# Kernel tuning notes

Measured on AMD Instinct MI355X. Metric: run time of the kernel, lower is better.

## Reference

```python
import jax, jax.numpy as jnp
import numpy as np

KH = KW = 3
K = KH * KW
STRIDE = 1
PAD = 1
DIL = 1
DG = 1  # deformable groups


def conv2d(x, w, b):
    out = jax.lax.conv_general_dilated(
        x, w, window_strides=(STRIDE, STRIDE),
        padding=[(PAD, PAD), (PAD, PAD)], rhs_dilation=(DIL, DIL),
        dimension_numbers=('NCHW', 'OIHW', 'NCHW'))
    return out + b[None, :, None, None]


def deform_conv2d(x, offset, mask, w, b):
    """DCNv2: bilinear sample at predicted offsets, modulate by mask, GEMM with w."""
    B, Cin, H, W = x.shape
    Ho, Wo = offset.shape[2], offset.shape[3]
    cpg = Cin // DG
    # torchvision layout: channel 2*(g*K+k) = dy, 2*(g*K+k)+1 = dx
    off = offset.reshape(B, DG, K, 2, Ho, Wo)
    off_y, off_x = off[:, :, :, 0], off[:, :, :, 1]  # [B,DG,K,Ho,Wo]
    m = mask.reshape(B, DG, K, Ho, Wo)
    ky = jnp.repeat(jnp.arange(KH), KW) * DIL          # [K] kernel row offsets
    kx = jnp.tile(jnp.arange(KW), KH) * DIL            # [K] kernel col offsets
    hh = jnp.arange(Ho) * STRIDE - PAD
    ww = jnp.arange(Wo) * STRIDE - PAD
    py = off_y + ky[None, None, :, None, None] + hh[None, None, None, :, None]
    px = off_x + kx[None, None, :, None, None] + ww[None, None, None, None, :]
    y0 = jnp.floor(py); x0 = jnp.floor(px)
    wy = py - y0; wx = px - x0
    x_g = x.reshape(B, DG, cpg, H * W)

    def gather(yc, xc):  # zero-padded bilinear corner fetch
        valid = ((yc >= 0) & (yc < H) & (xc >= 0) & (xc < W)).astype(x.dtype)
        yi = jnp.clip(yc, 0, H - 1).astype(jnp.int32)
        xi = jnp.clip(xc, 0, W - 1).astype(jnp.int32)
        idx = (yi * W + xi).reshape(B, DG, 1, K * Ho * Wo)
        v = jnp.take_along_axis(x_g, jnp.broadcast_to(idx, (B, DG, cpg, K * Ho * Wo)), axis=3)
        return v.reshape(B, DG, cpg, K, Ho, Wo) * valid[:, :, None]

    v00 = gather(y0, x0)
    v01 = gather(y0, x0 + 1)
    v10 = gather(y0 + 1, x0)
    v11 = gather(y0 + 1, x0 + 1)
    wy_b = wy[:, :, None]; wx_b = wx[:, :, None]  # broadcast over cpg
    sampled = (v00 * (1 - wy_b) * (1 - wx_b) + v01 * (1 - wy_b) * wx_b
               + v10 * wy_b * (1 - wx_b) + v11 * wy_b * wx_b)
    sampled = (sampled * m[:, :, None]).reshape(B, Cin, K, Ho, Wo)
    Cout = w.shape[0]
    out = jnp.einsum('bckhw,ock->bohw', sampled, w.reshape(Cout, Cin, K))
    return out + b[None, :, None, None]


def setup_inputs() -> dict:
    key = jax.random.key(0)
    k1, k2, k3, k4 = jax.random.split(key, 4)
    B, Cin, Cout, H, W = 8, 128, 128, 64, 64
    omc = DG * 3 * K  # 2*K offsets + K mask channels = 27
    x = jax.random.normal(k1, (B, Cin, H, W), dtype=jnp.float32)
    # small offset-conv weights -> modest predicted offsets (mimics near-zero init)
    w_off = jax.random.normal(k2, (omc, Cin, KH, KW), dtype=jnp.float32) * 0.01
    b_off = jnp.zeros((omc,), dtype=jnp.float32)
    w_def = jax.random.normal(k3, (Cout, Cin, KH, KW), dtype=jnp.float32) * (1.0 / np.sqrt(Cin * K))
    b_def = jax.random.normal(k4, (Cout,), dtype=jnp.float32) * 0.01
    return {"x": x, "w_off": w_off, "b_off": b_off, "w_def": w_def, "b_def": b_def}


def reference(x, w_off, b_off, w_def, b_def):
    out = conv2d(x, w_off, b_off)
    oc = DG * 2 * K
    offset = out[:, :oc]
    mask = jax.nn.sigmoid(out[:, oc:])
    return deform_conv2d(x, offset, mask, w_def, b_def)
```

## Files before the change

### kernel.cpp

```cpp
#include <hip/hip_runtime.h>
#include <math.h>

typedef _Float16 f16;
typedef __attribute__((ext_vector_type(2))) _Float16 f16x2;
typedef __attribute__((ext_vector_type(8))) _Float16 f16x8;
typedef __attribute__((ext_vector_type(4))) float f32x4;

#define NBATCH 8
#define WSA_ELE 36864
#define WSB_ELE 147456
#define OFF_WSB  73728
#define OFF_XT   368640

__device__ __forceinline__ void gload_lds16(const f16* gsrc, f16* ldst) {
  __builtin_amdgcn_global_load_lds(
      (const __attribute__((address_space(1))) unsigned int*)gsrc,
      (__attribute__((address_space(3))) unsigned int*)ldst, 16, 0, 0);
}

__global__ __launch_bounds__(256) void prep_w_kernel(const float* __restrict__ w_off,
                                                     const float* __restrict__ w_def,
                                                     f16* __restrict__ wsA,
                                                     f16* __restrict__ wsB) {
  int i = blockIdx.x * 256 + threadIdx.x;
  if (i < WSA_ELE) {
    int j = i & 7, lane = (i >> 3) & 63, fm = i >> 9;
    int ch = fm >> 1, mt = fm & 1;
    int row = mt * 16 + (lane & 15);
    int kidx = ch * 32 + (lane >> 4) * 8 + j;
    int k = kidx >> 7, cc = kidx & 127;
    float v = (row < 27) ? w_off[row * 1152 + cc * 9 + k] : 0.0f;
    wsA[i] = (f16)v;
  } else {
    int e = i - WSA_ELE;
    int j = e & 7, lane = (e >> 3) & 63, fm = e >> 9;
    int ch = fm >> 3, mt = fm & 7;
    int row = mt * 16 + (lane & 15);
    int kidx = ch * 32 + (lane >> 4) * 8 + j;
    int k = kidx >> 7, cc = kidx & 127;
    wsB[e] = (f16)w_def[row * 1152 + cc * 9 + k];
  }
}

__global__ __launch_bounds__(256) void transpose_kernel(const float* __restrict__ x,
                                                        f16* __restrict__ xt) {
  __shared__ f16 s_t[128 * 66];
  const int t = threadIdx.x;
  const int b = blockIdx.x >> 6;
  const int pos0 = (blockIdx.x & 63) << 6;
  const float* xb = x + ((size_t)b << 19);
  for (int i = t; i < 8192; i += 256) {
    int c = i >> 6, p = i & 63;
    s_t[c * 66 + p] = (f16)xb[c * 4096 + pos0 + p];
  }
  __syncthreads();
  f16* xtb = xt + ((size_t)b << 19);
  for (int i = t; i < 4096; i += 256) {
    int p = i >> 6, c2 = (i & 63) * 2;
    unsigned v0 = *(const unsigned short*)&s_t[c2 * 66 + p];
    unsigned v1 = *(const unsigned short*)&s_t[(c2 + 1) * 66 + p];
    *(unsigned*)&xtb[(size_t)(pos0 + p) * 128 + c2] = v0 | (v1 << 16);
  }
}

__global__ __launch_bounds__(256) void fused_dcn_kernel(const f16* __restrict__ xt,
                                                        const f16* __restrict__ wsA,
                                                        const f16* __restrict__ wsB,
                                                        const float* __restrict__ b_off,
                                                        const float* __restrict__ b_def,
                                                        float* __restrict__ out) {
  __shared__ float  s_off[27 * 65];
  __shared__ uint4  s_ofs[576];
  __shared__ float4 s_wt[576];
  __shared__ __align__(16) f16 s_a[2][4096];
  const int t = threadIdx.x;
  const int b = blockIdx.x >> 6, ho = blockIdx.x & 63;
  const int lane = t & 63, wid = t >> 6;
  const int q = lane >> 4, li = lane & 15;
  const int px = (wid << 4) + li;
  const char* xtb = (const char*)xt + ((size_t)b << 20);

  {
    const int seg = wid * 2;
    gload_lds16(wsB + seg * 512 + lane * 8,       &s_a[0][seg * 512]);
    gload_lds16(wsB + (seg + 1) * 512 + lane * 8, &s_a[0][(seg + 1) * 512]);
  }

  {
    f32x4 acc0 = {0.f, 0.f, 0.f, 0.f}, acc1 = {0.f, 0.f, 0.f, 0.f};
    for (int k = 0; k < 9; ++k) {
      const int ky = k / 3, kx = k - ky * 3;
      const int y = ho + ky - 1;
      const int xx = px + kx - 1;
      const bool valid = ((unsigned)y < 64u) && ((unsigned)xx < 64u);
      const int pos = min(max(y, 0), 63) * 64 + min(max(xx, 0), 63);
      const int voff = pos * 256 + q * 16;
      #pragma unroll
      for (int c4 = 0; c4 < 4; ++c4) {
        union { uint4 u; f16x8 v; } bu;
        bu.u = *(const uint4*)(xtb + voff + c4 * 64);
        if (!valid) { bu.u.x = 0u; bu.u.y = 0u; bu.u.z = 0u; bu.u.w = 0u; }
        const int ch = k * 4 + c4;
        f16x8 a0 = *(const f16x8*)&wsA[(ch * 2    ) * 512 + lane * 8];
        f16x8 a1 = *(const f16x8*)&wsA[(ch * 2 + 1) * 512 + lane * 8];
        acc0 = __builtin_amdgcn_mfma_f32_16x16x32_f16(a0, bu.v, acc0, 0, 0, 0);
        acc1 = __builtin_amdgcn_mfma_f32_16x16x32_f16(a1, bu.v, acc1, 0, 0, 0);
      }
    }
    #pragma unroll
    for (int mt = 0; mt < 2; ++mt) {
      f32x4 a = mt ? acc1 : acc0;
      #pragma unroll
      for (int r = 0; r < 4; ++r) {
        int oc = mt * 16 + q * 4 + r;
        if (oc < 27) {
          float v = a[r] + b_off[oc];
          if (oc >= 18) v = 1.0f / (1.0f + __expf(-v));
          s_off[oc * 65 + px] = v;
        }
      }
    }
  }
  __syncthreads();

  for (int f = t; f < 576; f += 256) {
    int k = f >> 6, p = f & 63;
    int ky = k / 3, kx = k - ky * 3;
    float oy = s_off[(2 * k    ) * 65 + p];
    float ox = s_off[(2 * k + 1) * 65 + p];
    float m  = s_off[(18 + k   ) * 65 + p];
    float py  = oy + (float)(ho + ky - 1);
    float pxf = ox + (float)(p + kx - 1);
    float y0f = floorf(py), x0f = floorf(pxf);
    float wy = py - y0f, wx = pxf - x0f;
    int y0 = (int)y0f, x0 = (int)x0f;
    int y1 = y0 + 1, x1 = x0 + 1;
    bool y0v = (unsigned)y0 < 64u, y1v = (unsigned)y1 < 64u;
    bool x0v = (unsigned)x0 < 64u, x1v = (unsigned)x1 < 64u;
    int y0c = min(max(y0, 0), 63), y1c = min(max(y1, 0), 63);
    int x0c = min(max(x0, 0), 63), x1c = min(max(x1, 0), 63);
    uint4 o4;
    o4.x = (unsigned)((y0c * 64 + x0c) * 256);
    o4.y = (unsigned)((y0c * 64 + x1c) * 256);
    o4.z = (unsigned)((y1c * 64 + x0c) * 256);
    o4.w = (unsigned)((y1c * 64 + x1c) * 256);
    float4 w4;
    w4.x = (y0v && x0v) ? (1.f - wy) * (1.f - wx) * m : 0.f;
    w4.y = (y0v && x1v) ? (1.f - wy) * wx         * m : 0.f;
    w4.z = (y1v && x0v) ? wy         * (1.f - wx) * m : 0.f;
    w4.w = (y1v && x1v) ? wy         * wx         * m : 0.f;
    s_ofs[f] = o4;
    s_wt[f]  = w4;
  }
  __syncthreads();

  f32x4 acc[8];
  #pragma unroll
  for (int mt = 0; mt < 8; ++mt) acc[mt] = (f32x4){0.f, 0.f, 0.f, 0.f};

  union U4 { uint4 u; f16x2 h[4]; };
  U4 d0c, d1c, d2c, d3c;

  {
    const uint4 o4 = s_ofs[px];
    d0c.u = *(const uint4*)(xtb + o4.x + q * 16);
    d1c.u = *(const uint4*)(xtb + o4.y + q * 16);
    d2c.u = *(const uint4*)(xtb + o4.z + q * 16);
    d3c.u = *(const uint4*)(xtb + o4.w + q * 16);
  }

  #pragma unroll 1
  for (int ch = 0; ch < 36; ++ch) {
    const int k = ch >> 2;
    if (ch < 35) {
      const int nb = (ch + 1) & 1;
      const int seg = wid * 2;
      const f16* src = wsB + (ch + 1) * 4096;
      gload_lds16(src + seg * 512 + lane * 8,       &s_a[nb][seg * 512]);
      gload_lds16(src + (seg + 1) * 512 + lane * 8, &s_a[nb][(seg + 1) * 512]);
    }
    U4 d0n, d1n, d2n, d3n;
    if (ch < 35) {
      const int kn = (ch + 1) >> 2, c4n = (ch + 1) & 3;
      const uint4 o4n = s_ofs[kn * 64 + px];
      const unsigned add = q * 16 + c4n * 64;
      d0n.u = *(const uint4*)(xtb + o4n.x + add);
      d1n.u = *(const uint4*)(xtb + o4n.y + add);
      d2n.u = *(const uint4*)(xtb + o4n.z + add);
      d3n.u = *(const uint4*)(xtb + o4n.w + add);
    }
    const float4 w4 = s_wt[k * 64 + px];
    const f16 h0 = (f16)w4.x, h1 = (f16)w4.y, h2 = (f16)w4.z, h3 = (f16)w4.w;
    const f16x2 wp0 = {h0, h0}, wp1 = {h1, h1}, wp2 = {h2, h2}, wp3 = {h3, h3};
    union { f16x2 h[4]; f16x8 v; } bf;
    #pragma unroll
    for (int i = 0; i < 4; ++i) {
      f16x2 s = d0c.h[i] * wp0;
      s = s + d1c.h[i] * wp1;
      s = s + d2c.h[i] * wp2;
      s = s + d3c.h[i] * wp3;
      bf.h[i] = s;
    }
    const f16* ab = &s_a[ch & 1][0];
    #pragma unroll
    for (int mt = 0; mt < 8; ++mt) {
      f16x8 a = *(const f16x8*)&ab[(mt * 64 + lane) * 8];
      acc[mt] = __builtin_amdgcn_mfma_f32_16x16x32_f16(a, bf.v, acc[mt], 0, 0, 0);
    }
    __syncthreads();
    if (ch < 35) { d0c = d0n; d1c = d1n; d2c = d2n; d3c = d3n; }
  }

  float* o = out + (size_t)b * 128 * 4096 + ho * 64 + px;
  #pragma unroll
  for (int mt = 0; mt < 8; ++mt) {
    #pragma unroll
    for (int r = 0; r < 4; ++r) {
      int oc = mt * 16 + q * 4 + r;
      o[oc * 4096] = acc[mt][r] + b_def[oc];
    }
  }
}

extern "C" void kernel_launch(void* const* d_in, const int* in_sizes, int n_in,
                              void* d_out, int out_size, void* d_ws, size_t ws_size,
                              hipStream_t stream) {
  const float* x     = (const float*)d_in[0];
  const float* w_off = (const float*)d_in[1];
  const float* b_off = (const float*)d_in[2];
  const float* w_def = (const float*)d_in[3];
  const float* b_def = (const float*)d_in[4];
  float* out = (float*)d_out;

  f16* wsA = (f16*)d_ws;
  f16* wsB = (f16*)((char*)d_ws + OFF_WSB);
  f16* xt  = (f16*)((char*)d_ws + OFF_XT);

  prep_w_kernel<<<dim3((WSA_ELE + WSB_ELE) / 256), dim3(256), 0, stream>>>(w_off, w_def, wsA, wsB);
  transpose_kernel<<<dim3(NBATCH * 64), dim3(256), 0, stream>>>(x, xt);
  fused_dcn_kernel<<<dim3(NBATCH * 64), dim3(256), 0, stream>>>(xt, wsA, wsB, b_off, b_def, out);
}
```

Before: 131.3 us.

## Merge weight prep and transpose kernels, vectorize transpose, reorder block mapping

Combines the weight-repacking and input-transpose kernels into one launch, with the first blocks doing weight prep and the rest doing the transpose, to save a kernel launch and its gap. The transpose now uses float4 global loads and 4-wide half stores with a padded LDS stride of 68. The main kernel's block index is remapped so consecutive blocks span batches rather than rows, which changes L2 locality. The offset-conv k loop is also fully unrolled, which may raise register pressure.

```diff
diff --git a/kernel.cpp b/kernel.cpp
--- a/kernel.cpp
+++ b/kernel.cpp
@@ -3,12 +3,14 @@
 
 typedef _Float16 f16;
 typedef __attribute__((ext_vector_type(2))) _Float16 f16x2;
+typedef __attribute__((ext_vector_type(4))) _Float16 f16x4;
 typedef __attribute__((ext_vector_type(8))) _Float16 f16x8;
 typedef __attribute__((ext_vector_type(4))) float f32x4;
 
 #define NBATCH 8
 #define WSA_ELE 36864
 #define WSB_ELE 147456
+#define PREP_BLOCKS 720
 #define OFF_WSB  73728
 #define OFF_XT   368640
 
@@ -18,48 +20,58 @@
       (__attribute__((address_space(3))) unsigned int*)ldst, 16, 0, 0);
 }
 
-__global__ __launch_bounds__(256) void prep_w_kernel(const float* __restrict__ w_off,
-                                                     const float* __restrict__ w_def,
-                                                     f16* __restrict__ wsA,
-                                                     f16* __restrict__ wsB) {
-  int i = blockIdx.x * 256 + threadIdx.x;
-  if (i < WSA_ELE) {
-    int j = i & 7, lane = (i >> 3) & 63, fm = i >> 9;
-    int ch = fm >> 1, mt = fm & 1;
-    int row = mt * 16 + (lane & 15);
-    int kidx = ch * 32 + (lane >> 4) * 8 + j;
-    int k = kidx >> 7, cc = kidx & 127;
-    float v = (row < 27) ? w_off[row * 1152 + cc * 9 + k] : 0.0f;
-    wsA[i] = (f16)v;
-  } else {
-    int e = i - WSA_ELE;
-    int j = e & 7, lane = (e >> 3) & 63, fm = e >> 9;
-    int ch = fm >> 3, mt = fm & 7;
-    int row = mt * 16 + (lane & 15);
-    int kidx = ch * 32 + (lane >> 4) * 8 + j;
-    int k = kidx >> 7, cc = kidx & 127;
-    wsB[e] = (f16)w_def[row * 1152 + cc * 9 + k];
-  }
-}
-
-__global__ __launch_bounds__(256) void transpose_kernel(const float* __restrict__ x,
-                                                        f16* __restrict__ xt) {
-  __shared__ f16 s_t[128 * 66];
+__global__ __launch_bounds__(256) void prep_transpose_kernel(const float* __restrict__ w_off,
+                                                             const float* __restrict__ w_def,
+                                                             f16* __restrict__ wsA,
+                                                             f16* __restrict__ wsB,
+                                                             const float* __restrict__ x,
+                                                             f16* __restrict__ xt) {
+  __shared__ __align__(16) f16 s_t[128 * 68];
   const int t = threadIdx.x;
-  const int b = blockIdx.x >> 6;
-  const int pos0 = (blockIdx.x & 63) << 6;
+  if (blockIdx.x < PREP_BLOCKS) {
+    int i = blockIdx.x * 256 + t;
+    if (i < WSA_ELE) {
+      int j = i & 7, lane = (i >> 3) & 63, fm = i >> 9;
+      int ch = fm >> 1, mt = fm & 1;
+      int row = mt * 16 + (lane & 15);
+      int kidx = ch * 32 + (lane >> 4) * 8 + j;
+      int k = kidx >> 7, cc = kidx & 127;
+      float v = (row < 27) ? w_off[row * 1152 + cc * 9 + k] : 0.0f;
+      wsA[i] = (f16)v;
+    } else {
+      int e = i - WSA_ELE;
+      int j = e & 7, lane = (e >> 3) & 63, fm = e >> 9;
+      int ch = fm >> 3, mt = fm & 7;
+      int row = mt * 16 + (lane & 15);
+      int kidx = ch * 32 + (lane >> 4) * 8 + j;
+      int k = kidx >> 7, cc = kidx & 127;
+      wsB[e] = (f16)w_def[row * 1152 + cc * 9 + k];
+    }
+    return;
+  }
+  const int bid = blockIdx.x - PREP_BLOCKS;
+  const int b = bid >> 6;
+  const int pos0 = (bid & 63) << 6;
   const float* xb = x + ((size_t)b << 19);
-  for (int i = t; i < 8192; i += 256) {
-    int c = i >> 6, p = i & 63;
-    s_t[c * 66 + p] = (f16)xb[c * 4096 + pos0 + p];
+  #pragma unroll
+  for (int it = 0; it < 8; ++it) {
+    int i = it * 256 + t;
+    int c = i >> 4, p4 = (i & 15) << 2;
+    float4 v = *(const float4*)&xb[c * 4096 + pos0 + p4];
+    f16x4 h = {(f16)v.x, (f16)v.y, (f16)v.z, (f16)v.w};
+    *(f16x4*)&s_t[c * 68 + p4] = h;
   }
   __syncthreads();
   f16* xtb = xt + ((size_t)b << 19);
-  for (int i = t; i < 4096; i += 256) {
-    int p = i >> 6, c2 = (i & 63) * 2;
-    unsigned v0 = *(const unsigned short*)&s_t[c2 * 66 + p];
-    unsigned v1 = *(const unsigned short*)&s_t[(c2 + 1) * 66 + p];
-    *(unsigned*)&xtb[(size_t)(pos0 + p) * 128 + c2] = v0 | (v1 << 16);
+  #pragma unroll
+  for (int it = 0; it < 8; ++it) {
+    int i = it * 256 + t;
+    int p = i >> 5, c4 = (i & 31) << 2;
+    f16x4 h = {s_t[(c4    ) * 68 + p],
+               s_t[(c4 + 1) * 68 + p],
+               s_t[(c4 + 2) * 68 + p],
+               s_t[(c4 + 3) * 68 + p]};
+    *(f16x4*)&xtb[(size_t)(pos0 + p) * 128 + c4] = h;
   }
 }
 
@@ -74,7 +86,7 @@
   __shared__ float4 s_wt[576];
   __shared__ __align__(16) f16 s_a[2][4096];
   const int t = threadIdx.x;
-  const int b = blockIdx.x >> 6, ho = blockIdx.x & 63;
+  const int b = blockIdx.x & 7, ho = blockIdx.x >> 3;
   const int lane = t & 63, wid = t >> 6;
   const int q = lane >> 4, li = lane & 15;
   const int px = (wid << 4) + li;
@@ -88,6 +100,7 @@
 
   {
     f32x4 acc0 = {0.f, 0.f, 0.f, 0.f}, acc1 = {0.f, 0.f, 0.f, 0.f};
+    #pragma unroll
     for (int k = 0; k < 9; ++k) {
       const int ky = k / 3, kx = k - ky * 3;
       const int y = ho + ky - 1;
@@ -236,7 +249,7 @@
   f16* wsB = (f16*)((char*)d_ws + OFF_WSB);
   f16* xt  = (f16*)((char*)d_ws + OFF_XT);
 
-  prep_w_kernel<<<dim3((WSA_ELE + WSB_ELE) / 256), dim3(256), 0, stream>>>(w_off, w_def, wsA, wsB);
-  transpose_kernel<<<dim3(NBATCH * 64), dim3(256), 0, stream>>>(x, xt);
+  prep_transpose_kernel<<<dim3(PREP_BLOCKS + NBATCH * 64), dim3(256), 0, stream>>>(
+      w_off, w_def, wsA, wsB, x, xt);
   fused_dcn_kernel<<<dim3(NBATCH * 64), dim3(256), 0, stream>>>(xt, wsA, wsB, b_off, b_def, out);
 }
```

After: 128.0 us. 1.03x faster.
